# Kernel optimization log

Measured on AMD Instinct MI355X. Metric: run time of the kernel, lower is better.

## Reference

```python
import jax, jax.numpy as jnp
import numpy as np
from jax import lax

K = 3        # kernel_size
G = 2        # group
STRIDE = 2
PAD = K // 2
EPS = 1e-5


def setup_inputs() -> dict:
    key = jax.random.key(0)
    k1, k2 = jax.random.split(key)
    x = jax.random.normal(k1, (4, 64, 256, 256), dtype=jnp.float32)
    # kaiming_normal_ fan_out relu: std = sqrt(2 / (out_ch * k * k))
    std = np.sqrt(2.0 / (G * K * K * K * K))
    conv_w = jax.random.normal(k2, (G * K * K, 64, K, K), dtype=jnp.float32) * std
    gamma = jnp.ones((G * K * K,), dtype=jnp.float32)
    beta = jnp.zeros((G * K * K,), dtype=jnp.float32)
    return {"x": x, "conv_w": conv_w, "gamma": gamma, "beta": beta}


def reference(x, conv_w, gamma, beta):
    n, c, h, w = x.shape
    # reflect pad (k//2 on each side)
    x_pad = jnp.pad(x, ((0, 0), (0, 0), (PAD, PAD), (PAD, PAD)), mode='reflect')
    # sigma = conv(pad(x)) -> [n, G*K*K, h, w]
    sigma = lax.conv_general_dilated(
        x_pad, conv_w, window_strides=(1, 1), padding='VALID',
        dimension_numbers=('NCHW', 'OIHW', 'NCHW'))
    # BatchNorm2d, training-mode forward (batch stats, biased var)
    mean = sigma.mean(axis=(0, 2, 3))
    var = sigma.var(axis=(0, 2, 3))
    sigma = (sigma - mean[None, :, None, None]) * (
        gamma[None, :, None, None] * lax.rsqrt(var + EPS)[None, :, None, None]
    ) + beta[None, :, None, None]
    # softmax over ALL g*k^2 channels (as in the torch code: Softmax(dim=1))
    sigma = jax.nn.softmax(sigma, axis=1)
    sigma = sigma.reshape(n, G, K * K, h, w)          # channel = g*K*K + k
    # unfold: k*k shifted views of the padded input -> [n, c, K*K, h, w]
    patches = jnp.stack(
        [x_pad[:, :, i:i + h, j:j + w] for i in range(K) for j in range(K)],
        axis=2)
    patches = patches.reshape(n, G, c // G, K * K, h, w)
    # per-pixel adaptive kernel aggregation, shared kernel within each group
    out = jnp.einsum('ngckhw,ngkhw->ngchw', patches, sigma).reshape(n, c, h, w)
    # strided subsampling (indices where idx % stride == 0)
    return out[:, :, ::STRIDE, ::STRIDE]
```

## Files before the change

### kernel.cpp

```cpp
#include <hip/hip_runtime.h>

typedef short bf16x8 __attribute__((ext_vector_type(8)));
typedef float f32x16 __attribute__((ext_vector_type(16)));

#define CIN 64
#define OC 18
#define NB 4
#define H 256
#define W 256
#define HW (H * W)
#define OH 128
#define OW 128
#define EPS 1e-5f

#define TSX 16
#define TSY 8
#define NTILE 4
#define WPX 36
#define ROWW (18 * WPX)
#define AWORDS (10 * ROWW)
#define NWB 512


__device__ __forceinline__ int refl(int i, int n) {
    if (i < 0) i = -i;
    if (i >= n) i = 2 * n - 2 - i;
    return i;
}

__device__ __forceinline__ unsigned pack_bf16(float a, float b) {
    __bf16 lo = (__bf16)a, hi = (__bf16)b;
    return (unsigned)__builtin_bit_cast(unsigned short, lo) |
           ((unsigned)__builtin_bit_cast(unsigned short, hi) << 16);
}

__global__ __launch_bounds__(256) void nhwc_kernel(
        const float* __restrict__ x, uint4* __restrict__ xt,
        const float* __restrict__ wgt, uint4* __restrict__ wB)
{
    if (blockIdx.y == NB) {
        if (blockIdx.x < 9) {
            int idx = blockIdx.x * 256 + threadIdx.x;
            int s = idx >> 6, l = idx & 63;
            int tap = s >> 2, ci0 = (s & 3) * 16;
            int oc = l & 31, kg = l >> 5;
            unsigned r[4];
#pragma unroll
            for (int jp = 0; jp < 4; jp++) {
                float v0 = 0.f, v1 = 0.f;
                int ci = ci0 + kg * 8 + jp * 2;
                if (oc < OC) {
                    v0 = wgt[(oc * CIN + ci) * 9 + tap];
                    v1 = wgt[(oc * CIN + ci + 1) * 9 + tap];
                }
                r[jp] = pack_bf16(v0, v1);
            }
            wB[idx] = make_uint4(r[0], r[1], r[2], r[3]);
        }
        return;
    }

    __shared__ uint4 bufq[2048];
    unsigned* buf = (unsigned*)bufq;

    const int h = blockIdx.x, n = blockIdx.y;
    const int t = threadIdx.x;
    const int tpx = t & 63;
    const int cg = t >> 6;
    const int px0 = tpx * 4;
    const unsigned swz = ((unsigned)tpx & 7u) << 2;

    const float* xrow = x + ((size_t)n * CIN * H + h) * W;

#pragma unroll
    for (int ii = 0; ii < 4; ii++) {
        const int cq = cg * 4 + ii;
        const float4 A0 = *(const float4*)(xrow + (size_t)(4 * cq + 0) * HW + px0);
        const float4 A1 = *(const float4*)(xrow + (size_t)(4 * cq + 1) * HW + px0);
        const float4 A2 = *(const float4*)(xrow + (size_t)(4 * cq + 2) * HW + px0);
        const float4 A3 = *(const float4*)(xrow + (size_t)(4 * cq + 3) * HW + px0);
        const float a0[4] = {A0.x, A0.y, A0.z, A0.w};
        const float a1[4] = {A1.x, A1.y, A1.z, A1.w};
        const float a2[4] = {A2.x, A2.y, A2.z, A2.w};
        const float a3[4] = {A3.x, A3.y, A3.z, A3.w};
#pragma unroll
        for (int i = 0; i < 4; i++) {
            unsigned lo = pack_bf16(a0[i], a1[i]);
            unsigned hi = pack_bf16(a2[i], a3[i]);
            unsigned widx = (unsigned)(px0 + i) * 32u + ((unsigned)(2 * cq) ^ swz);
            *(uint2*)&buf[widx] = make_uint2(lo, hi);
        }
    }
    __syncthreads();

    const size_t rowbase = ((size_t)(n * H + h)) * W * 8;
#pragma unroll
    for (int i = 0; i < 8; i++) {
        int flat = i * 256 + t;
        int px = flat >> 3, j = flat & 7;
        unsigned sw = (((unsigned)px >> 2) & 7u) << 2;
        uint4 v = *(const uint4*)&buf[(unsigned)px * 32u + (((unsigned)(4 * j)) ^ sw)];
        xt[rowbase + flat] = v;
    }
}

__global__ __launch_bounds__(256, 2) void conv_kernel(
        const uint4* __restrict__ xt, const uint4* __restrict__ wB,
        float* __restrict__ sigma_s, float* __restrict__ part)
{
    __shared__ unsigned alds[3][AWORDS];
    __shared__ float sred[2 * OC];

    const int tid = threadIdx.x;
    const int lane = tid & 63;

    const int b = blockIdx.x;
    const int cls = b & 7;
    const int L = b >> 3;
    const int n = cls >> 1;
    const int hhalf = cls & 1;
    const int ht = L >> 2;
    const int wq = L & 3;
    const int h0 = (hhalf * 16 + ht) * TSY;
    const int w0 = wq * (NTILE * TSX);

    if (tid < 2 * OC) sred[tid] = 0.f;

    uint4 breg[36];
#pragma unroll
    for (int s = 0; s < 36; s++) breg[s] = wB[s * 64 + lane];

    size_t gbase[6];
    int    alw[6], apx[6];
    bool   av[6];
#pragma unroll
    for (int i = 0; i < 6; i++) {
        int e = tid + i * 256;
        av[i] = e < 1440;
        if (!av[i]) e = 1439;
        int row = e / 144;
        int rr  = e - row * 144;
        int px  = rr >> 3;
        int c   = rr & 7;
        int gh  = refl(h0 + row - 1, H);
        gbase[i] = (size_t)(n * H + gh) * W * 8 + c;
        apx[i]  = px;
        alw[i]  = row * ROWW + px * WPX + c * 4;
    }

    {
        uint4 ast[6];
#pragma unroll
        for (int i = 0; i < 6; i++) {
            if (av[i]) {
                int gw = refl(w0 + apx[i] - 1, W);
                ast[i] = xt[gbase[i] + (size_t)gw * 8];
            }
        }
#pragma unroll
        for (int i = 0; i < 6; i++)
            if (av[i]) *(uint4*)&alds[0][alw[i]] = ast[i];
    }
    __syncthreads();

    const int wv = tid >> 6;
    const int m = lane & 31;
    const int kg = lane >> 5;
    const int pr = m >> 4, pc = m & 15;
    const int r0 = 2 * wv + pr;
    const int abase = r0 * ROWW + pc * WPX + kg * 4;

    float s_acc = 0.f, ss_acc = 0.f;
    const int oy = (h0 >> 1) + wv;
    const size_t pb_n = (size_t)n * OC;

#pragma unroll 1
    for (int t = 0; t < NTILE; t++) {
        uint4 pfa[6];
        if (t + 1 < NTILE) {
            const int w0n = w0 + (t + 1) * TSX;
#pragma unroll
            for (int i = 0; i < 6; i++) {
                if (av[i]) {
                    int gw = refl(w0n + apx[i] - 1, W);
                    pfa[i] = xt[gbase[i] + (size_t)gw * 8];
                }
            }
        }

        const unsigned* ap = &alds[t % 3][abase];
        f32x16 acc = {};
#pragma unroll
        for (int g = 0; g < 9; g++) {
            const int kh = g / 3, kw = g % 3;
#pragma unroll
            for (int q = 0; q < 4; q++) {
                uint4 af = *(const uint4*)(ap + kh * ROWW + kw * WPX + q * 8);
                acc = __builtin_amdgcn_mfma_f32_32x32x16_bf16(
                        __builtin_bit_cast(bf16x8, af),
                        __builtin_bit_cast(bf16x8, breg[g * 4 + q]), acc, 0, 0, 0);
            }
        }

#pragma unroll
        for (int rr = 0; rr < 16; rr++) {
            s_acc  += acc[rr];
            ss_acc += acc[rr] * acc[rr];
        }
        if (m < OC) {
            const int ox0 = (w0 + t * TSX) >> 1;
            const size_t pbase = ((pb_n + m) * OH + oy) * OW;
#pragma unroll
            for (int rr = 0; rr < 16; rr++) {
                int p = (rr & 3) + 8 * (rr >> 2) + 4 * kg;
                if (p < 16 && (p & 1) == 0)
                    sigma_s[pbase + ox0 + (p >> 1)] = acc[rr];
            }
        }

        if (t + 1 < NTILE) {
#pragma unroll
            for (int i = 0; i < 6; i++)
                if (av[i]) *(uint4*)&alds[(t + 1) % 3][alw[i]] = pfa[i];
        }
        __syncthreads();
    }

    s_acc  += __shfl_xor(s_acc, 32);
    ss_acc += __shfl_xor(ss_acc, 32);
    if (kg == 0 && m < OC) {
        atomicAdd(&sred[m], s_acc);
        atomicAdd(&sred[OC + m], ss_acc);
    }
    __syncthreads();
    if (tid < 2 * OC) part[tid * NWB + blockIdx.x] = sred[tid];
}

__global__ __launch_bounds__(256) void bn_kernel(
        const float* __restrict__ gamma, const float* __restrict__ beta,
        const float* __restrict__ part, float* __restrict__ stats)
{
    __shared__ float red[8];
    const int c = blockIdx.x;
    const int tid = threadIdx.x;

    float s  = part[c * NWB + tid]        + part[c * NWB + 256 + tid];
    float ss = part[(OC + c) * NWB + tid] + part[(OC + c) * NWB + 256 + tid];
#pragma unroll
    for (int off = 32; off > 0; off >>= 1) {
        s  += __shfl_down(s, off);
        ss += __shfl_down(ss, off);
    }
    const int wid = tid >> 6, lanez = tid & 63;
    if (lanez == 0) { red[wid] = s; red[4 + wid] = ss; }
    __syncthreads();
    if (tid == 0) {
        float S  = red[0] + red[1] + red[2] + red[3];
        float SS = red[4] + red[5] + red[6] + red[7];
        float cnt = (float)NB * H * W;
        float mean = S / cnt;
        float var  = SS / cnt - mean * mean;
        float sc   = gamma[c] * rsqrtf(var + EPS);
        stats[36 + c] = sc;
        stats[54 + c] = beta[c] - mean * sc;
    }
}

__global__ __launch_bounds__(256) void out_kernel(
        const uint4* __restrict__ xt, const float* __restrict__ sigma_s,
        const float* __restrict__ stats, float* __restrict__ out)
{
    __shared__ float p_lds[OC][64];

    const int oh = blockIdx.x;
    const int n  = blockIdx.y >> 1;
    const int ow0 = (blockIdx.y & 1) * 64;
    const int h  = 2 * oh;
    const int tid = threadIdx.x;

    for (int i = tid; i < OC * 64; i += 256) {
        int ch = i >> 6, owl = i & 63;
        float v = sigma_s[((size_t)(n * OC + ch) * OH + oh) * OW + ow0 + owl];
        p_lds[ch][owl] = v * stats[36 + ch] + stats[54 + ch];
    }
    __syncthreads();

    if (tid < 64) {
        int owl = tid;
        float mx = -1e30f;
#pragma unroll
        for (int ch = 0; ch < OC; ch++) mx = fmaxf(mx, p_lds[ch][owl]);
        float e[OC], sum = 0.f;
#pragma unroll
        for (int ch = 0; ch < OC; ch++) { e[ch] = __expf(p_lds[ch][owl] - mx); sum += e[ch]; }
        float inv = 1.f / sum;
#pragma unroll
        for (int ch = 0; ch < OC; ch++) p_lds[ch][owl] = e[ch] * inv;
    }
    __syncthreads();

    int ihs[3];
#pragma unroll
    for (int kh = 0; kh < 3; kh++) ihs[kh] = refl(h - 1 + kh, H);

#pragma unroll
    for (int it = 0; it < 2; it++) {
        const int flat = it * 256 + tid;
        const int c8 = flat & 7;
        const int owl = flat >> 3;
        const int ow = ow0 + owl;
        const int g = (c8 >= 4) ? 1 : 0;

        float a[8];
#pragma unroll
        for (int j = 0; j < 8; j++) a[j] = 0.f;

#pragma unroll
        for (int kh = 0; kh < 3; kh++) {
            const size_t rb = ((size_t)(n * H + ihs[kh])) * W * 8;
#pragma unroll
            for (int kw = 0; kw < 3; kw++) {
                const int iw = refl(2 * ow - 1 + kw, W);
                const float p = p_lds[g * 9 + kh * 3 + kw][owl];
                uint4 v = xt[rb + (size_t)iw * 8 + c8];
                const unsigned uu[4] = {v.x, v.y, v.z, v.w};
#pragma unroll
                for (int q = 0; q < 4; q++) {
                    float lo = __builtin_bit_cast(float, uu[q] << 16);
                    float hi = __builtin_bit_cast(float, uu[q] & 0xffff0000u);
                    a[2 * q]     = fmaf(p, lo, a[2 * q]);
                    a[2 * q + 1] = fmaf(p, hi, a[2 * q + 1]);
                }
            }
        }

        const size_t ob = ((size_t)(n * CIN + c8 * 8) * OH + oh) * OW + ow;
#pragma unroll
        for (int j = 0; j < 8; j++)
            out[ob + (size_t)j * OH * OW] = a[j];
    }
}

extern "C" void kernel_launch(void* const* d_in, const int* in_sizes, int n_in,
                              void* d_out, int out_size, void* d_ws, size_t ws_size,
                              hipStream_t stream) {
    const float* x     = (const float*)d_in[0];
    const float* cw    = (const float*)d_in[1];
    const float* gamma = (const float*)d_in[2];
    const float* beta  = (const float*)d_in[3];
    float* out = (float*)d_out;
    float* ws  = (float*)d_ws;

    float* stats   = ws;
    float* sigma_s = ws + 256;
    uint4* wBp     = (uint4*)(sigma_s + (size_t)NB * OC * OH * OW);
    uint4* xtp     = wBp + 36 * 64;
    float* part    = (float*)(xtp + (size_t)NB * H * W * 8);

    dim3 gT(H, NB + 1);
    nhwc_kernel<<<gT, 256, 0, stream>>>(x, xtp, cw, wBp);

    conv_kernel<<<dim3(NWB), 256, 0, stream>>>(xtp, wBp, sigma_s, part);

    bn_kernel<<<OC, 256, 0, stream>>>(gamma, beta, part, stats);

    dim3 gC(OH, NB * 2);
    out_kernel<<<gC, 256, 0, stream>>>(xtp, sigma_s, stats, out);
}
```

Baseline: 62.21 us.

## Fuse BN stats finalize into conv via last-block counter; store sigma pixel-major

Removes the separate bn_kernel launch: each conv block increments a global counter after writing its partial sums, and the last block reduces all partials and writes the BN scale and shift. The counter is zeroed in the transpose kernel. Sigma storage changes from channel-major to pixel-major (18 channels contiguous per pixel), so the out kernel reads it contiguously into a padded LDS layout. This saves one launch and makes the sigma loads coalesced, at the cost of scattered 4-byte stores in conv and a serial tail reduction inside one conv block.

```diff
diff --git a/kernel.cpp b/kernel.cpp
--- a/kernel.cpp
+++ b/kernel.cpp
@@ -36,7 +36,8 @@
 
 __global__ __launch_bounds__(256) void nhwc_kernel(
         const float* __restrict__ x, uint4* __restrict__ xt,
-        const float* __restrict__ wgt, uint4* __restrict__ wB)
+        const float* __restrict__ wgt, uint4* __restrict__ wB,
+        unsigned* __restrict__ cnt)
 {
     if (blockIdx.y == NB) {
         if (blockIdx.x < 9) {
@@ -56,6 +57,8 @@
                 r[jp] = pack_bf16(v0, v1);
             }
             wB[idx] = make_uint4(r[0], r[1], r[2], r[3]);
+        } else if (blockIdx.x == 9 && threadIdx.x == 0) {
+            *cnt = 0;
         }
         return;
     }
@@ -106,10 +109,13 @@
 
 __global__ __launch_bounds__(256, 2) void conv_kernel(
         const uint4* __restrict__ xt, const uint4* __restrict__ wB,
-        float* __restrict__ sigma_s, float* __restrict__ part)
+        float* __restrict__ sigma_s, float* __restrict__ part,
+        float* __restrict__ stats, const float* __restrict__ gamma,
+        const float* __restrict__ beta, unsigned* __restrict__ cnt)
 {
     __shared__ unsigned alds[3][AWORDS];
     __shared__ float sred[2 * OC];
+    __shared__ unsigned lastv;
 
     const int tid = threadIdx.x;
     const int lane = tid & 63;
@@ -172,7 +178,7 @@
 
     float s_acc = 0.f, ss_acc = 0.f;
     const int oy = (h0 >> 1) + wv;
-    const size_t pb_n = (size_t)n * OC;
+    const size_t orow = ((size_t)n * OH + oy) * OW;
 
 #pragma unroll 1
     for (int t = 0; t < NTILE; t++) {
@@ -207,14 +213,13 @@
             s_acc  += acc[rr];
             ss_acc += acc[rr] * acc[rr];
         }
+
         if (m < OC) {
             const int ox0 = (w0 + t * TSX) >> 1;
-            const size_t pbase = ((pb_n + m) * OH + oy) * OW;
-#pragma unroll
-            for (int rr = 0; rr < 16; rr++) {
-                int p = (rr & 3) + 8 * (rr >> 2) + 4 * kg;
-                if (p < 16 && (p & 1) == 0)
-                    sigma_s[pbase + ox0 + (p >> 1)] = acc[rr];
+#pragma unroll
+            for (int rr = 0; rr < 8; rr += 2) {
+                int p2 = ((rr & 3) >> 1) + 4 * (rr >> 2) + 2 * kg;
+                sigma_s[(orow + ox0 + p2) * OC + m] = acc[rr];
             }
         }
 
@@ -234,35 +239,38 @@
     }
     __syncthreads();
     if (tid < 2 * OC) part[tid * NWB + blockIdx.x] = sred[tid];
-}
-
-__global__ __launch_bounds__(256) void bn_kernel(
-        const float* __restrict__ gamma, const float* __restrict__ beta,
-        const float* __restrict__ part, float* __restrict__ stats)
-{
-    __shared__ float red[8];
-    const int c = blockIdx.x;
-    const int tid = threadIdx.x;
-
-    float s  = part[c * NWB + tid]        + part[c * NWB + 256 + tid];
-    float ss = part[(OC + c) * NWB + tid] + part[(OC + c) * NWB + 256 + tid];
-#pragma unroll
-    for (int off = 32; off > 0; off >>= 1) {
-        s  += __shfl_down(s, off);
-        ss += __shfl_down(ss, off);
-    }
-    const int wid = tid >> 6, lanez = tid & 63;
-    if (lanez == 0) { red[wid] = s; red[4 + wid] = ss; }
-    __syncthreads();
-    if (tid == 0) {
-        float S  = red[0] + red[1] + red[2] + red[3];
-        float SS = red[4] + red[5] + red[6] + red[7];
-        float cnt = (float)NB * H * W;
-        float mean = S / cnt;
-        float var  = SS / cnt - mean * mean;
-        float sc   = gamma[c] * rsqrtf(var + EPS);
-        stats[36 + c] = sc;
-        stats[54 + c] = beta[c] - mean * sc;
+
+    __threadfence();
+    __syncthreads();
+    if (tid == 0) lastv = atomicAdd(cnt, 1u);
+    __syncthreads();
+    if (lastv == NWB - 1) {
+        __threadfence();
+        const int wid = tid >> 6, lz = tid & 63;
+#pragma unroll 1
+        for (int c = 0; c < OC; c++) {
+            float s = part[c * NWB + tid]        + part[c * NWB + 256 + tid];
+            float q = part[(OC + c) * NWB + tid] + part[(OC + c) * NWB + 256 + tid];
+#pragma unroll
+            for (int off = 32; off > 0; off >>= 1) {
+                s += __shfl_down(s, off);
+                q += __shfl_down(q, off);
+            }
+            if (lz == 0) { sred[wid] = s; sred[4 + wid] = q; }
+            __syncthreads();
+            if (tid == 0) {
+                float S = sred[0] + sred[1] + sred[2] + sred[3];
+                float Q = sred[4] + sred[5] + sred[6] + sred[7];
+                float cf = (float)NB * H * W;
+                float mean = S / cf;
+                float var  = Q / cf - mean * mean;
+                float sc   = gamma[c] * rsqrtf(var + EPS);
+                stats[36 + c] = sc;
+                stats[54 + c] = beta[c] - mean * sc;
+            }
+            __syncthreads();
+        }
+        if (tid == 0) *cnt = 0;
     }
 }
 
@@ -270,7 +278,7 @@
         const uint4* __restrict__ xt, const float* __restrict__ sigma_s,
         const float* __restrict__ stats, float* __restrict__ out)
 {
-    __shared__ float p_lds[OC][64];
+    __shared__ float p_lds[64 * 19];
 
     const int oh = blockIdx.x;
     const int n  = blockIdx.y >> 1;
@@ -278,24 +286,24 @@
     const int h  = 2 * oh;
     const int tid = threadIdx.x;
 
-    for (int i = tid; i < OC * 64; i += 256) {
-        int ch = i >> 6, owl = i & 63;
-        float v = sigma_s[((size_t)(n * OC + ch) * OH + oh) * OW + ow0 + owl];
-        p_lds[ch][owl] = v * stats[36 + ch] + stats[54 + ch];
+    const float* srow = sigma_s + ((size_t)(n * OH + oh) * OW + ow0) * OC;
+    for (int i = tid; i < 64 * OC; i += 256) {
+        int owl = i / OC, ch = i - owl * OC;
+        p_lds[owl * 19 + ch] = srow[i] * stats[36 + ch] + stats[54 + ch];
     }
     __syncthreads();
 
     if (tid < 64) {
-        int owl = tid;
+        float* pr = &p_lds[tid * 19];
         float mx = -1e30f;
 #pragma unroll
-        for (int ch = 0; ch < OC; ch++) mx = fmaxf(mx, p_lds[ch][owl]);
+        for (int ch = 0; ch < OC; ch++) mx = fmaxf(mx, pr[ch]);
         float e[OC], sum = 0.f;
 #pragma unroll
-        for (int ch = 0; ch < OC; ch++) { e[ch] = __expf(p_lds[ch][owl] - mx); sum += e[ch]; }
+        for (int ch = 0; ch < OC; ch++) { e[ch] = __expf(pr[ch] - mx); sum += e[ch]; }
         float inv = 1.f / sum;
 #pragma unroll
-        for (int ch = 0; ch < OC; ch++) p_lds[ch][owl] = e[ch] * inv;
+        for (int ch = 0; ch < OC; ch++) pr[ch] = e[ch] * inv;
     }
     __syncthreads();
 
@@ -310,6 +318,7 @@
         const int owl = flat >> 3;
         const int ow = ow0 + owl;
         const int g = (c8 >= 4) ? 1 : 0;
+        const float* pr = &p_lds[owl * 19 + g * 9];
 
         float a[8];
 #pragma unroll
@@ -321,7 +330,7 @@
 #pragma unroll
             for (int kw = 0; kw < 3; kw++) {
                 const int iw = refl(2 * ow - 1 + kw, W);
-                const float p = p_lds[g * 9 + kh * 3 + kw][owl];
+                const float p = pr[kh * 3 + kw];
                 uint4 v = xt[rb + (size_t)iw * 8 + c8];
                 const unsigned uu[4] = {v.x, v.y, v.z, v.w};
 #pragma unroll
@@ -351,18 +360,18 @@
     float* out = (float*)d_out;
     float* ws  = (float*)d_ws;
 
-    float* stats   = ws;
-    float* sigma_s = ws + 256;
-    uint4* wBp     = (uint4*)(sigma_s + (size_t)NB * OC * OH * OW);
-    uint4* xtp     = wBp + 36 * 64;
-    float* part    = (float*)(xtp + (size_t)NB * H * W * 8);
+    float*    stats   = ws;
+    unsigned* cnt     = (unsigned*)(ws + 128);
+    float*    sigma_s = ws + 256;
+    uint4*    wBp     = (uint4*)(sigma_s + (size_t)NB * OH * OW * OC);
+    uint4*    xtp     = wBp + 36 * 64;
+    float*    part    = (float*)(xtp + (size_t)NB * H * W * 8);
 
     dim3 gT(H, NB + 1);
-    nhwc_kernel<<<gT, 256, 0, stream>>>(x, xtp, cw, wBp);
-
-    conv_kernel<<<dim3(NWB), 256, 0, stream>>>(xtp, wBp, sigma_s, part);
-
-    bn_kernel<<<OC, 256, 0, stream>>>(gamma, beta, part, stats);
+    nhwc_kernel<<<gT, 256, 0, stream>>>(x, xtp, cw, wBp, cnt);
+
+    conv_kernel<<<dim3(NWB), 256, 0, stream>>>(xtp, wBp, sigma_s, part,
+                                               stats, gamma, beta, cnt);
 
     dim3 gC(OH, NB * 2);
     out_kernel<<<gC, 256, 0, stream>>>(xtp, sigma_s, stats, out);
```

Result: slower. 118.9 us (+91.1%).
